# Optimization experiments

Hardware: AMD Instinct MI355X
Metric: run time of the kernel (lower is better)

## Reference

```python
import jax, jax.numpy as jnp
import numpy as np

B, C, W, H, HEADS = 32, 512, 32, 32, 8
D = C // HEADS
N = W * H
LN_EPS = 1e-5


def setup_inputs() -> dict:
    key = jax.random.key(0)
    ks = jax.random.split(key, 11)
    s = 1.0 / np.sqrt(C)
    return {
        "x": jax.random.normal(ks[0], (B, C, W, H), jnp.float32),
        "Wq": jax.random.normal(ks[1], (C, C), jnp.float32) * s,
        "bq": jax.random.normal(ks[2], (C,), jnp.float32) * 0.01,
        "Wk": jax.random.normal(ks[3], (C, C), jnp.float32) * s,
        "bk": jax.random.normal(ks[4], (C,), jnp.float32) * 0.01,
        "Wv": jax.random.normal(ks[5], (C, C), jnp.float32) * s,
        "bv": jax.random.normal(ks[6], (C,), jnp.float32) * 0.01,
        "rel_h": jax.random.normal(ks[7], (1, HEADS, D, 1, H), jnp.float32),
        "rel_w": jax.random.normal(ks[8], (1, HEADS, D, W, 1), jnp.float32),
        "ln_w": jnp.ones((C, W, H), jnp.float32),
        "ln_b": jnp.zeros((C, W, H), jnp.float32),
    }


def reference(x, Wq, bq, Wk, bk, Wv, bv, rel_h, rel_w, ln_w, ln_b):
    b, c, w, h = x.shape
    nh, d, n = HEADS, c // HEADS, w * h

    def proj(Wm, bm):
        # 1x1 conv == per-pixel linear: out[b,o,w,h] = sum_c Wm[o,c] x[b,c,w,h] + bm[o]
        y = jnp.einsum('bcwh,oc->bowh', x, Wm) + bm[None, :, None, None]
        return y.reshape(b, nh, d, n)

    q = proj(Wq, bq)  # [B,h,d,N]
    k = proj(Wk, bk)
    v = proj(Wv, bv)

    # content-content: q^T k -> [B,h,N,N]
    cc = jnp.einsum('bhdn,bhdm->bhnm', q, k)
    # content-position: (rel_h + rel_w) flattened to [h,d,N], permuted, matmul with q
    pos = (rel_h + rel_w).reshape(nh, d, n)  # [h,d,N]
    cp = jnp.einsum('hdn,bhdm->bhnm', pos, q)

    attn = jax.nn.softmax(cc + cp, axis=-1)  # [B,h,N,N]
    # out = v @ attn^T  -> [B,h,d,N]
    out = jnp.einsum('bhdn,bhmn->bhdm', v, attn)
    out = out.reshape(b, c, w, h)

    # LayerNorm over [C,W,H] with elementwise affine, then residual
    mu = jnp.mean(out, axis=(1, 2, 3), keepdims=True)
    var = jnp.var(out, axis=(1, 2, 3), keepdims=True)
    out = (out - mu) * jax.lax.rsqrt(var + LN_EPS) * ln_w[None] + ln_b[None]
    return out + x
```

## Files before the change

kernel.cpp:

```cpp
#include <hip/hip_runtime.h>
#include <stdint.h>

typedef _Float16 f16x8 __attribute__((ext_vector_type(8)));
typedef _Float16 f16x4 __attribute__((ext_vector_type(4)));
typedef __fp16   fp16x2 __attribute__((ext_vector_type(2)));
typedef float f32x4  __attribute__((ext_vector_type(4)));

__device__ __forceinline__ _Float16 f2h(float f){ return (_Float16)f; }

#define NB   32
#define NC   512
#define NH   8
#define ND   64
#define NN   1024

#define LOG2E 1.44269504f

__global__ __launch_bounds__(256) void wt_conv(const float* __restrict__ Wq,
                                               const float* __restrict__ Wk,
                                               const float* __restrict__ Wv,
                                               _Float16* __restrict__ Wt){
  int idx = blockIdx.x * 256 + threadIdx.x;
  int sel = idx >> 18;
  const float* W = (sel == 0) ? Wq : (sel == 1) ? Wk : Wv;
  Wt[idx] = f2h(W[idx & 262143]);
}

__global__ __launch_bounds__(256) void transpose_x(const float* __restrict__ x,
                                                   _Float16* __restrict__ xT){
  __shared__ float tile[32][33];
  int n0 = blockIdx.x * 32, c0 = blockIdx.y * 32, b = blockIdx.z;
  int t = threadIdx.x;
  int tn = t & 31, tc = t >> 5;
#pragma unroll
  for (int k = 0; k < 4; k++)
    tile[tc + 8*k][tn] = x[(b*NC + c0 + tc + 8*k)*NN + n0 + tn];
  __syncthreads();
#pragma unroll
  for (int k = 0; k < 4; k++)
    xT[(b*NN + n0 + tc + 8*k)*NC + c0 + tn] = f2h(tile[tn][tc + 8*k]);
}

__global__ __launch_bounds__(256) void pos_conv(const float* __restrict__ rel_h,
                                                const float* __restrict__ rel_w,
                                                _Float16* __restrict__ pos_t){
  int idx = blockIdx.x * 256 + threadIdx.x;
  int d = idx & 63, n = (idx >> 6) & 1023, h = idx >> 16;
  int ww = n >> 5, hh = n & 31;
  float v = rel_h[(h*ND + d)*32 + hh] + rel_w[(h*ND + d)*32 + ww];
  pos_t[idx] = f2h(v);
}

#define ASTR 72
#define TSTR 136

__global__ __launch_bounds__(256) void proj_gemm(const _Float16* __restrict__ Wt,
                                                 const _Float16* __restrict__ xT,
                                                 const float* __restrict__ bq,
                                                 const float* __restrict__ bk,
                                                 const float* __restrict__ bv,
                                                 _Float16* __restrict__ q_ws,
                                                 _Float16* __restrict__ k_ws,
                                                 _Float16* __restrict__ v_ws){
  __shared__ _Float16 smem[2 * 128 * ASTR];
  _Float16* As = smem;
  _Float16* Bs = smem + 128 * ASTR;

  int mt = blockIdx.x;
  int nt = blockIdx.y;
  int b  = blockIdx.z;
  int t = threadIdx.x, lane = t & 63, w = t >> 6;
  int wm = w >> 1, wn = w & 1;
  int lr = lane & 15, lg = lane >> 4;

  f32x4 acc[4][4];
#pragma unroll
  for (int i = 0; i < 4; i++)
#pragma unroll
    for (int j = 0; j < 4; j++) acc[i][j] = (f32x4)0.f;

  const _Float16* Arow = Wt + mt * 128 * NC;
  const _Float16* Brow = xT + (b * NN + nt * 128) * NC;

  for (int k0 = 0; k0 < NC; k0 += 64){
    __syncthreads();
#pragma unroll
    for (int i = 0; i < 4; i++){
      int lin = t + 256 * i;
      int row = lin >> 3, c8 = lin & 7;
      *(f16x8*)(As + row*ASTR + c8*8) = *(const f16x8*)(Arow + row*NC + k0 + c8*8);
      *(f16x8*)(Bs + row*ASTR + c8*8) = *(const f16x8*)(Brow + row*NC + k0 + c8*8);
    }
    __syncthreads();
#pragma unroll
    for (int ks = 0; ks < 2; ks++){
      f16x8 af[4], bfr[4];
#pragma unroll
      for (int mi = 0; mi < 4; mi++)
        af[mi] = *(f16x8*)(As + (wm*64 + mi*16 + lr)*ASTR + ks*32 + lg*8);
#pragma unroll
      for (int nj = 0; nj < 4; nj++)
        bfr[nj] = *(f16x8*)(Bs + (wn*64 + nj*16 + lr)*ASTR + ks*32 + lg*8);
#pragma unroll
      for (int mi = 0; mi < 4; mi++)
#pragma unroll
        for (int nj = 0; nj < 4; nj++)
          acc[mi][nj] = __builtin_amdgcn_mfma_f32_16x16x32_f16(af[mi], bfr[nj], acc[mi][nj], 0, 0, 0);
    }
  }
  __syncthreads();

  if (mt < 8){
    _Float16* Ts = smem;
#pragma unroll
    for (int mi = 0; mi < 4; mi++){
      int o0 = wm*64 + mi*16 + 4*lg;
      int og = mt*128 + o0;
      int sel = og >> 9, oo = og & 511;
      const float* bias = (sel == 0) ? bq : bk;
      float sc = (sel == 0) ? LOG2E : 1.f;
      float b0 = bias[oo], b1 = bias[oo+1], b2 = bias[oo+2], b3 = bias[oo+3];
#pragma unroll
      for (int nj = 0; nj < 4; nj++){
        int pix = wn*64 + nj*16 + lr;
        f16x4 pk;
        pk[0] = f2h((acc[mi][nj][0] + b0) * sc);
        pk[1] = f2h((acc[mi][nj][1] + b1) * sc);
        pk[2] = f2h((acc[mi][nj][2] + b2) * sc);
        pk[3] = f2h((acc[mi][nj][3] + b3) * sc);
        *(f16x4*)(Ts + pix*TSTR + o0) = pk;
      }
    }
    __syncthreads();
#pragma unroll
    for (int i = 0; i < 8; i++){
      int lin = t + 256 * i;
      int c_o = lin & 15, pix = lin >> 4;
      f16x8 v = *(f16x8*)(Ts + pix*TSTR + c_o*8);
      int og = mt*128 + c_o*8;
      int sel = og >> 9, oo = og & 511;
      int head = oo >> 6, d = oo & 63;
      _Float16* dst = (sel == 0) ? q_ws : k_ws;
      *(f16x8*)(dst + (((b*NH + head)*NN) + nt*128 + pix)*ND + d) = v;
    }
  } else {
    _Float16* Ts2 = smem;
#pragma unroll
    for (int mi = 0; mi < 4; mi++){
      int o0 = wm*64 + mi*16 + 4*lg;
      int vb = (mt - 8)*128 + o0;
      float b0 = bv[vb], b1 = bv[vb+1], b2 = bv[vb+2], b3 = bv[vb+3];
#pragma unroll
      for (int nj = 0; nj < 4; nj++){
        int pix = wn*64 + nj*16 + lr;
        Ts2[(o0+0)*TSTR + pix] = f2h(acc[mi][nj][0] + b0);
        Ts2[(o0+1)*TSTR + pix] = f2h(acc[mi][nj][1] + b1);
        Ts2[(o0+2)*TSTR + pix] = f2h(acc[mi][nj][2] + b2);
        Ts2[(o0+3)*TSTR + pix] = f2h(acc[mi][nj][3] + b3);
      }
    }
    __syncthreads();
#pragma unroll
    for (int i = 0; i < 8; i++){
      int lin = t + 256 * i;
      int pix8 = lin & 15, o_loc = lin >> 4;
      f16x8 v = *(f16x8*)(Ts2 + o_loc*TSTR + pix8*8);
      int vb = (mt - 8)*128 + o_loc;
      int head = vb >> 6, d = vb & 63;
      *(f16x8*)(v_ws + ((b*NH + head)*ND + d)*NN + nt*128 + pix8*8) = v;
    }
  }
}

#define KSTR 136
#define OFF_VT 8704

__global__ __launch_bounds__(256) void attn_kernel(const _Float16* __restrict__ q_ws,
                                                   const _Float16* __restrict__ k_ws,
                                                   const _Float16* __restrict__ v_ws,
                                                   const _Float16* __restrict__ pos_t,
                                                   float* __restrict__ out,
                                                   float* __restrict__ red){
  __shared__ _Float16 smem[12800];
  __shared__ float lnred[8];
  _Float16* Kc = smem;
  _Float16* Vt = smem + OFF_VT;

  int bid = blockIdx.x;
  int sid = (bid & 7) * 256 + (bid >> 3);
  int qt = sid & 7, h = (sid >> 3) & 7, b = sid >> 6;

  int t = threadIdx.x, lane = t & 63, w = t >> 6;
  int lr = lane & 15, lg = lane >> 4;

  const _Float16* qbh = q_ws + (b*NH + h) * NN * ND;
  const _Float16* kbh = k_ws + (b*NH + h) * NN * ND;
  const _Float16* vbh = v_ws + (b*NH + h) * ND * NN;
  const _Float16* pph = pos_t + h * NN * ND;

  f16x8 qreg[2][4];
#pragma unroll
  for (int qi = 0; qi < 2; qi++){
    int row = qt*128 + w*32 + qi*16 + lr;
#pragma unroll
    for (int ks = 0; ks < 4; ks++){
      const _Float16* src = (ks < 2) ? (qbh + row*ND + ks*32 + lg*8)
                                     : (pph + row*ND + (ks-2)*32 + lg*8);
      qreg[qi][ks] = *(const f16x8*)src;
    }
  }

  int k_row = t >> 4, k_c8 = t & 15;
  int v_d0 = t >> 3, v_ch = t & 7;

  float m_r[2], l_r[2];
  f32x4 oacc[2][4];
#pragma unroll
  for (int qi = 0; qi < 2; qi++){ m_r[qi] = -1e30f; l_r[qi] = 0.f; }
#pragma unroll
  for (int qi = 0; qi < 2; qi++)
#pragma unroll
    for (int dj = 0; dj < 4; dj++) oacc[qi][dj] = (f32x4)0.f;

  union pfu { fp16x2 h2[4]; f16x8 v8; };
  union vfu { f16x4 v4[2]; f16x8 v8; };

  for (int n0 = 0; n0 < NN; n0 += 64){
    __syncthreads();
#pragma unroll
    for (int i = 0; i < 4; i++){
      int row = k_row + i*16;
      const _Float16* src = (k_c8 < 8) ? (kbh + (n0 + row)*ND + k_c8*8)
                                       : (qbh + (n0 + row)*ND + (k_c8 - 8)*8);
      *(f16x8*)(Kc + row*KSTR + k_c8*8) = *(const f16x8*)src;
    }
#pragma unroll
    for (int i = 0; i < 2; i++){
      int d = v_d0 + i*32;
      *(f16x8*)(Vt + d*64 + ((v_ch*8) ^ ((d & 7) << 3))) = *(const f16x8*)(vbh + d*NN + n0 + v_ch*8);
    }
    __syncthreads();

    f32x4 sacc[4][2];
#pragma unroll
    for (int kt = 0; kt < 4; kt++)
#pragma unroll
      for (int qi = 0; qi < 2; qi++) sacc[kt][qi] = (f32x4)0.f;
#pragma unroll
    for (int ks = 0; ks < 4; ks++){
      f16x8 kf[4];
#pragma unroll
      for (int kt = 0; kt < 4; kt++)
        kf[kt] = *(f16x8*)(Kc + (kt*16 + lr)*KSTR + ks*32 + lg*8);
#pragma unroll
      for (int kt = 0; kt < 4; kt++)
#pragma unroll
        for (int qi = 0; qi < 2; qi++)
          sacc[kt][qi] = __builtin_amdgcn_mfma_f32_16x16x32_f16(kf[kt], qreg[qi][ks], sacc[kt][qi], 0, 0, 0);
    }

    pfu pa[2][2];
#pragma unroll
    for (int qi = 0; qi < 2; qi++){
      float m0 = fmaxf(fmaxf(sacc[0][qi][0], sacc[0][qi][1]), fmaxf(sacc[0][qi][2], sacc[0][qi][3]));
      float m1 = fmaxf(fmaxf(sacc[1][qi][0], sacc[1][qi][1]), fmaxf(sacc[1][qi][2], sacc[1][qi][3]));
      float m2 = fmaxf(fmaxf(sacc[2][qi][0], sacc[2][qi][1]), fmaxf(sacc[2][qi][2], sacc[2][qi][3]));
      float m3 = fmaxf(fmaxf(sacc[3][qi][0], sacc[3][qi][1]), fmaxf(sacc[3][qi][2], sacc[3][qi][3]));
      float mx = fmaxf(fmaxf(m0, m1), fmaxf(m2, m3));
      mx = fmaxf(mx, __shfl_xor(mx, 16));
      mx = fmaxf(mx, __shfl_xor(mx, 32));
      if (!__all(mx - m_r[qi] <= 11.f)){
        float mn2 = fmaxf(m_r[qi], mx);
        float cr = __builtin_exp2f(m_r[qi] - mn2);
        m_r[qi] = mn2;
        l_r[qi] *= cr;
#pragma unroll
        for (int dj = 0; dj < 4; dj++) oacc[qi][dj] *= cr;
      }
      float mn = m_r[qi];
      float ts = 0.f;
#pragma unroll
      for (int kt = 0; kt < 4; kt++){
        float p0 = __builtin_exp2f(sacc[kt][qi][0] - mn);
        float p1 = __builtin_exp2f(sacc[kt][qi][1] - mn);
        float p2 = __builtin_exp2f(sacc[kt][qi][2] - mn);
        float p3 = __builtin_exp2f(sacc[kt][qi][3] - mn);
        ts += (p0 + p1) + (p2 + p3);
        pa[qi][kt >> 1].h2[((kt & 1) << 1) + 0] = __builtin_amdgcn_cvt_pkrtz(p0, p1);
        pa[qi][kt >> 1].h2[((kt & 1) << 1) + 1] = __builtin_amdgcn_cvt_pkrtz(p2, p3);
      }
      ts += __shfl_xor(ts, 16);
      ts += __shfl_xor(ts, 32);
      l_r[qi] += ts;
    }

#pragma unroll
    for (int ks = 0; ks < 2; ks++){
      f16x8 vf[4];
#pragma unroll
      for (int dj = 0; dj < 4; dj++){
        int row = dj*16 + lr;
        int sw = (row & 7) << 3;
        vfu u;
        u.v4[0] = *(f16x4*)(Vt + row*64 + ((ks*32 + lg*4) ^ sw));
        u.v4[1] = *(f16x4*)(Vt + row*64 + ((ks*32 + 16 + lg*4) ^ sw));
        vf[dj] = u.v8;
      }
#pragma unroll
      for (int qi = 0; qi < 2; qi++)
#pragma unroll
        for (int dj = 0; dj < 4; dj++)
          oacc[qi][dj] = __builtin_amdgcn_mfma_f32_16x16x32_f16(vf[dj], pa[qi][ks].v8, oacc[qi][dj], 0, 0, 0);
    }
  }

  float s_ln = 0.f, q_ln = 0.f;
#pragma unroll
  for (int qi = 0; qi < 2; qi++){
    float iv = 1.f / l_r[qi];
    int qcol = qt*128 + w*32 + qi*16 + lr;
#pragma unroll
    for (int dj = 0; dj < 4; dj++){
#pragma unroll
      for (int r = 0; r < 4; r++){
        float val = oacc[qi][dj][r] * iv;
        s_ln += val; q_ln += val*val;
        out[(b*NC + h*ND + dj*16 + 4*lg + r)*NN + qcol] = val;
      }
    }
  }

#pragma unroll
  for (int off = 1; off < 64; off <<= 1){
    s_ln += __shfl_xor(s_ln, off);
    q_ln += __shfl_xor(q_ln, off);
  }
  if (lane == 0){ lnred[w*2] = s_ln; lnred[w*2 + 1] = q_ln; }
  __syncthreads();
  if (t == 0){
    int idx = ((b*NH + h)*8 + qt)*2;
    red[idx]     = lnred[0] + lnred[2] + lnred[4] + lnred[6];
    red[idx + 1] = lnred[1] + lnred[3] + lnred[5] + lnred[7];
  }
}

__global__ void ln_stats(const float* __restrict__ red, float* __restrict__ stats){
  int b = threadIdx.x;
  if (b < 32){
    float s = 0.f, sq = 0.f;
    for (int j = 0; j < 64; j++){ s += red[(b*64 + j)*2]; sq += red[(b*64 + j)*2 + 1]; }
    float mu  = s * (1.f / 524288.f);
    float var = sq * (1.f / 524288.f) - mu*mu;
    stats[b*2] = mu;
    stats[b*2 + 1] = rsqrtf(var + 1e-5f);
  }
}

__global__ __launch_bounds__(256) void ln_apply(const float* __restrict__ x,
                                                const float* __restrict__ lw,
                                                const float* __restrict__ lb,
                                                const float* __restrict__ stats,
                                                float* __restrict__ out){
  int tid = blockIdx.x*256 + threadIdx.x;
  for (int i4 = tid; i4 < 4194304; i4 += 524288){
    int b = i4 >> 17;
    int r4 = i4 & 131071;
    float mu = stats[b*2], rs = stats[b*2 + 1];
    float4 o  = ((const float4*)out)[i4];
    float4 xv = ((const float4*)x)[i4];
    float4 ww = ((const float4*)lw)[r4];
    float4 bb = ((const float4*)lb)[r4];
    o.x = (o.x - mu)*rs*ww.x + bb.x + xv.x;
    o.y = (o.y - mu)*rs*ww.y + bb.y + xv.y;
    o.z = (o.z - mu)*rs*ww.z + bb.z + xv.z;
    o.w = (o.w - mu)*rs*ww.w + bb.w + xv.w;
    ((float4*)out)[i4] = o;
  }
}

extern "C" void kernel_launch(void* const* d_in, const int* in_sizes, int n_in,
                              void* d_out, int out_size, void* d_ws, size_t ws_size,
                              hipStream_t stream){
  (void)in_sizes; (void)n_in; (void)out_size; (void)ws_size;
  const float* x    = (const float*)d_in[0];
  const float* Wq   = (const float*)d_in[1];
  const float* bq   = (const float*)d_in[2];
  const float* Wk   = (const float*)d_in[3];
  const float* bk   = (const float*)d_in[4];
  const float* Wv   = (const float*)d_in[5];
  const float* bv   = (const float*)d_in[6];
  const float* relh = (const float*)d_in[7];
  const float* relw = (const float*)d_in[8];
  const float* lnw  = (const float*)d_in[9];
  const float* lnb  = (const float*)d_in[10];
  float* out = (float*)d_out;
  char* ws = (char*)d_ws;

  _Float16* q_ws  = (_Float16*)(ws);
  _Float16* k_ws  = (_Float16*)(ws + 33554432);
  _Float16* v_ws  = (_Float16*)(ws + 67108864);
  _Float16* xT    = (_Float16*)(ws + 100663296);
  _Float16* Wt    = (_Float16*)(ws + 134217728);
  _Float16* pos_t = (_Float16*)(ws + 135790592);
  float* red   = (float*)(ws + 136839168);
  float* stats = red + 4096;

  wt_conv    <<<3072, 256, 0, stream>>>(Wq, Wk, Wv, Wt);
  transpose_x<<<dim3(32, 16, 32), 256, 0, stream>>>(x, xT);
  pos_conv   <<<2048, 256, 0, stream>>>(relh, relw, pos_t);
  proj_gemm  <<<dim3(12, 8, 32), 256, 0, stream>>>(Wt, xT, bq, bk, bv, q_ws, k_ws, v_ws);
  attn_kernel<<<2048, 256, 0, stream>>>(q_ws, k_ws, v_ws, pos_t, out, red);
  ln_stats   <<<1, 64, 0, stream>>>(red, stats);
  ln_apply   <<<2048, 256, 0, stream>>>(x, lnw, lnb, stats, out);
}
```

Baseline: 340.6 us.

## Double-buffer attention K/Q/V tiles via direct global-to-LDS async loads

Replaces the register-staged K/Q/V tile copy in the attention loop with global_load_lds direct-to-LDS loads into a double buffer. The next tile is prefetched while the current one is computed, and the barriers drop from two per iteration to one. The LDS layout changes from a padded stride to an XOR-swizzled 64-wide layout, with the read addressing updated to match. LDS use roughly doubles, which may lower occupancy, and the correctness of the swizzle depends on how global_load_lds places each lane's data.

```diff
diff --git a/kernel.cpp b/kernel.cpp
--- a/kernel.cpp
+++ b/kernel.cpp
@@ -7,6 +7,11 @@
 typedef float f32x4  __attribute__((ext_vector_type(4)));
 
 __device__ __forceinline__ _Float16 f2h(float f){ return (_Float16)f; }
+
+__device__ __forceinline__ void gl16(const void* g, void* l){
+  __builtin_amdgcn_global_load_lds((const __attribute__((address_space(1))) void*)g,
+                                   (__attribute__((address_space(3))) void*)l, 16, 0, 0);
+}
 
 #define NB   32
 #define NC   512
@@ -172,8 +177,7 @@
   }
 }
 
-#define KSTR 136
-#define OFF_VT 8704
+#define BUFH 12288
 
 __global__ __launch_bounds__(256) void attn_kernel(const _Float16* __restrict__ q_ws,
                                                    const _Float16* __restrict__ k_ws,
@@ -181,10 +185,8 @@
                                                    const _Float16* __restrict__ pos_t,
                                                    float* __restrict__ out,
                                                    float* __restrict__ red){
-  __shared__ _Float16 smem[12800];
+  __shared__ _Float16 smem[2*BUFH];
   __shared__ float lnred[8];
-  _Float16* Kc = smem;
-  _Float16* Vt = smem + OFF_VT;
 
   int bid = blockIdx.x;
   int sid = (bid & 7) * 256 + (bid >> 3);
@@ -210,8 +212,8 @@
     }
   }
 
-  int k_row = t >> 4, k_c8 = t & 15;
-  int v_d0 = t >> 3, v_ch = t & 7;
+  int s_row8 = lane >> 3;
+  int s_g    = lane & 7;
 
   float m_r[2], l_r[2];
   f32x4 oacc[2][4];
@@ -225,21 +227,30 @@
   union pfu { fp16x2 h2[4]; f16x8 v8; };
   union vfu { f16x4 v4[2]; f16x8 v8; };
 
-  for (int n0 = 0; n0 < NN; n0 += 64){
-    __syncthreads();
-#pragma unroll
-    for (int i = 0; i < 4; i++){
-      int row = k_row + i*16;
-      const _Float16* src = (k_c8 < 8) ? (kbh + (n0 + row)*ND + k_c8*8)
-                                       : (qbh + (n0 + row)*ND + (k_c8 - 8)*8);
-      *(f16x8*)(Kc + row*KSTR + k_c8*8) = *(const f16x8*)src;
-    }
-#pragma unroll
-    for (int i = 0; i < 2; i++){
-      int d = v_d0 + i*32;
-      *(f16x8*)(Vt + d*64 + ((v_ch*8) ^ ((d & 7) << 3))) = *(const f16x8*)(vbh + d*NN + n0 + v_ch*8);
-    }
-    __syncthreads();
+#define STAGE_TILE(bufp, n0s)                                                          \
+  do {                                                                                 \
+    _Float16* Kk_ = (bufp);                                                            \
+    _Float16* Kq_ = (bufp) + 4096;                                                     \
+    _Float16* Vt_ = (bufp) + 8192;                                                     \
+    _Pragma("unroll")                                                                  \
+    for (int j = 0; j < 2; j++){                                                       \
+      int r0  = w*16 + j*8;                                                            \
+      int row = r0 + s_row8;                                                           \
+      int gx  = (s_g ^ (row & 7)) << 3;                                                \
+      gl16(kbh + (n0s + row)*ND + gx, Kk_ + r0*64);                                    \
+      gl16(qbh + (n0s + row)*ND + gx, Kq_ + r0*64);                                    \
+      gl16(vbh + row*NN + (n0s) + gx, Vt_ + r0*64);                                    \
+    }                                                                                  \
+  } while (0)
+
+  STAGE_TILE(smem, 0);
+  __syncthreads();
+
+  for (int tt = 0; tt < 16; tt++){
+    _Float16* bb = smem + (tt & 1)*BUFH;
+    _Float16* Kk = bb, *Kq = bb + 4096, *Vt = bb + 8192;
+    if (tt < 15)
+      STAGE_TILE(smem + ((tt + 1) & 1)*BUFH, (tt + 1)*64);
 
     f32x4 sacc[4][2];
 #pragma unroll
@@ -247,16 +258,21 @@
 #pragma unroll
       for (int qi = 0; qi < 2; qi++) sacc[kt][qi] = (f32x4)0.f;
 #pragma unroll
-    for (int ks = 0; ks < 4; ks++){
-      f16x8 kf[4];
-#pragma unroll
-      for (int kt = 0; kt < 4; kt++)
-        kf[kt] = *(f16x8*)(Kc + (kt*16 + lr)*KSTR + ks*32 + lg*8);
-#pragma unroll
-      for (int kt = 0; kt < 4; kt++)
-#pragma unroll
-        for (int qi = 0; qi < 2; qi++)
-          sacc[kt][qi] = __builtin_amdgcn_mfma_f32_16x16x32_f16(kf[kt], qreg[qi][ks], sacc[kt][qi], 0, 0, 0);
+    for (int half = 0; half < 2; half++){
+      _Float16* Ksrc = half ? Kq : Kk;
+#pragma unroll
+      for (int ks = 0; ks < 2; ks++){
+        int xg = (((ks << 2) | lg) ^ (lr & 7)) << 3;
+        f16x8 kf[4];
+#pragma unroll
+        for (int kt = 0; kt < 4; kt++)
+          kf[kt] = *(f16x8*)(Ksrc + (kt*16 + lr)*64 + xg);
+#pragma unroll
+        for (int kt = 0; kt < 4; kt++)
+#pragma unroll
+          for (int qi = 0; qi < 2; qi++)
+            sacc[kt][qi] = __builtin_amdgcn_mfma_f32_16x16x32_f16(kf[kt], qreg[qi][half*2 + ks], sacc[kt][qi], 0, 0, 0);
+      }
     }
 
     pfu pa[2][2];
@@ -300,10 +316,13 @@
 #pragma unroll
       for (int dj = 0; dj < 4; dj++){
         int row = dj*16 + lr;
-        int sw = (row & 7) << 3;
+        int sw = row & 7;
+        int g0 = ((4*ks + (lg >> 1)) ^ sw) << 3;
+        int g1 = ((4*ks + 2 + (lg >> 1)) ^ sw) << 3;
+        int sub = (lg & 1) << 2;
         vfu u;
-        u.v4[0] = *(f16x4*)(Vt + row*64 + ((ks*32 + lg*4) ^ sw));
-        u.v4[1] = *(f16x4*)(Vt + row*64 + ((ks*32 + 16 + lg*4) ^ sw));
+        u.v4[0] = *(f16x4*)(Vt + row*64 + g0 + sub);
+        u.v4[1] = *(f16x4*)(Vt + row*64 + g1 + sub);
         vf[dj] = u.v8;
       }
 #pragma unroll
@@ -312,6 +331,8 @@
         for (int dj = 0; dj < 4; dj++)
           oacc[qi][dj] = __builtin_amdgcn_mfma_f32_16x16x32_f16(vf[dj], pa[qi][ks].v8, oacc[qi][dj], 0, 0, 0);
     }
+
+    __syncthreads();
   }
 
   float s_ln = 0.f, q_ln = 0.f;
```

Result: faster. 329.2 us (-3.3%).
